# Kernel optimization log

Measured on AMD Instinct MI355X. Metric: run time of the kernel, lower is better.

The kernel has to match this reference:

```python
import jax, jax.numpy as jnp
import numpy as np

B, T, D, UNITS = 32, 2048, 1024, 1024


def setup_inputs() -> dict:
    key = jax.random.key(0)
    ks = jax.random.split(key, 9)
    values = jax.random.normal(ks[0], (B, T, D), dtype=jnp.float32)
    query = jax.random.normal(ks[1], (B, D), dtype=jnp.float32)
    # mask: 1.0 where position is masked out, 0.0 otherwise
    mask = jax.random.randint(ks[2], (B, T), 0, 2).astype(jnp.float32)
    # Dense params (keras Dense: y = x @ W + b)
    W1 = jax.random.normal(ks[3], (D, UNITS), dtype=jnp.float32) / np.sqrt(D)
    b1 = jnp.zeros((UNITS,), dtype=jnp.float32)
    W2 = jax.random.normal(ks[4], (D, UNITS), dtype=jnp.float32) / np.sqrt(D)
    b2 = jnp.zeros((UNITS,), dtype=jnp.float32)
    V = jax.random.normal(ks[5], (UNITS, 1), dtype=jnp.float32) / np.sqrt(UNITS)
    bV = jnp.zeros((1,), dtype=jnp.float32)
    return {"values": values, "query": query, "mask": mask,
            "W1": W1, "b1": b1, "W2": W2, "b2": b2, "V": V, "bV": bV}


def reference(values, query, mask, W1, b1, W2, b2, V, bV):
    # values: [B,T,D], query: [B,D], mask: [B,T] (1.0 = masked)
    proj_v = jnp.einsum('btd,du->btu', values, W1) + b1          # [B,T,U]
    proj_q = (query @ W2 + b2)[:, None, :]                        # [B,1,U]
    score = jnp.tanh(proj_v + proj_q) @ V + bV                    # [B,T,1]
    score = score + mask[:, :, None] * (-1e9)                     # mask out
    attention_weights = jax.nn.softmax(score, axis=1)             # [B,T,1]
    context_vector = jnp.sum(attention_weights * values, axis=1)  # [B,D]
    return (context_vector, attention_weights)
```

## Files before the change

### kernel.cpp

```cpp
#include <hip/hip_runtime.h>
#include <hip/hip_bf16.h>


typedef __bf16 bf16x8 __attribute__((ext_vector_type(8)));
typedef __bf16 bf16x4 __attribute__((ext_vector_type(4)));
typedef float  f32x4  __attribute__((ext_vector_type(4)));

#define B_  32
#define T_  2048
#define D_  1024
#define U_  1024
#define BT_ (B_*T_)

#define WS_W1T    ((size_t)0)
#define WS_PROJQ  ((size_t)(2u*1024*1024))
#define WS_SCORE  ((size_t)(2u*1024*1024 + 128u*1024))
#define WS_VALB   ((size_t)(4u*1024*1024))
#define WS_NEEDED (WS_VALB + (size_t)BT_ * D_ * 2)

__device__ __forceinline__ float tanh_fast(float x) {
    const float e = __expf(2.0f * x);
    return 1.0f - __fdividef(2.0f, e + 1.0f);
}

__device__ __forceinline__ void glls16(const void* g, void* l) {
    __builtin_amdgcn_global_load_lds(
        (const __attribute__((address_space(1))) void*)g,
        (__attribute__((address_space(3))) void*)l, 16, 0, 0);
}

__global__ void init_kernel(const float* __restrict__ b1, const float* __restrict__ b2,
                            float* __restrict__ projq, float* __restrict__ score) {
    int i = blockIdx.x * 256 + threadIdx.x;
    if (i < B_ * U_) {
        projq[i] = b1[i & (U_ - 1)] + b2[i & (U_ - 1)];
    } else {
        score[i - B_ * U_] = 0.0f;
    }
}

__global__ void convert_kernel(const float* __restrict__ v, __bf16* __restrict__ o) {
    const size_t i = ((size_t)blockIdx.x * 256 + threadIdx.x) * 8;
    const float4 a = *(const float4*)(v + i);
    const float4 b = *(const float4*)(v + i + 4);
    bf16x8 h;
    h[0] = (__bf16)a.x; h[1] = (__bf16)a.y; h[2] = (__bf16)a.z; h[3] = (__bf16)a.w;
    h[4] = (__bf16)b.x; h[5] = (__bf16)b.y; h[6] = (__bf16)b.z; h[7] = (__bf16)b.w;
    *(bf16x8*)(o + i) = h;
}

__global__ void w1_transpose_kernel(const float* __restrict__ W1, __bf16* __restrict__ W1T) {
    __shared__ float tile[64][65];
    const int bx = blockIdx.x & 15;
    const int by = blockIdx.x >> 4;
    const int tid = threadIdx.x;
    const int j  = tid & 63;
    const int i0 = tid >> 6;
#pragma unroll
    for (int p = 0; p < 16; ++p) {
        const int i = i0 + p * 4;
        tile[i][j] = W1[(size_t)(by * 64 + i) * U_ + bx * 64 + j];
    }
    __syncthreads();
#pragma unroll
    for (int p = 0; p < 16; ++p) {
        const int i = i0 + p * 4;
        W1T[(size_t)(bx * 64 + i) * D_ + by * 64 + j] = (__bf16)tile[j][i];
    }
}

__global__ void projq_kernel(const float* __restrict__ query, const float* __restrict__ W2,
                             float* __restrict__ projq) {
    __shared__ float q[128];
    const int b  = blockIdx.x >> 3;
    const int dc = blockIdx.x & 7;
    const int tid = threadIdx.x;
    if (tid < 128) q[tid] = query[(size_t)b * D_ + dc * 128 + tid];
    __syncthreads();
    const int u0 = tid * 4;
    float a0 = 0.f, a1 = 0.f, a2 = 0.f, a3 = 0.f;
    for (int d = 0; d < 128; ++d) {
        const float4 w = *(const float4*)(W2 + (size_t)(dc * 128 + d) * U_ + u0);
        const float qd = q[d];
        a0 = fmaf(qd, w.x, a0); a1 = fmaf(qd, w.y, a1);
        a2 = fmaf(qd, w.z, a2); a3 = fmaf(qd, w.w, a3);
    }
    float* p = projq + (size_t)b * U_ + u0;
    atomicAdd(p + 0, a0); atomicAdd(p + 1, a1);
    atomicAdd(p + 2, a2); atomicAdd(p + 3, a3);
}


#define SC_A_ELE 4096
#define SC_B_ELE 8192
#define SC_BUF   (SC_A_ELE + SC_B_ELE)

__global__ __launch_bounds__(512, 4)
void score_kernel_occ(const __bf16* __restrict__ valb, const __bf16* __restrict__ W1T,
                      const float* __restrict__ projq, const float* __restrict__ V,
                      float* __restrict__ score) {
    __shared__ __attribute__((aligned(16))) __bf16 lds[2 * SC_BUF];

    const int tid  = threadIdx.x;
    const int bid  = blockIdx.x;
    const int xcd  = bid & 7;
    const int sl   = bid >> 3;
    const int mblk = xcd * 64 + (sl >> 2);
    const int nblk = sl & 3;

    const int wv   = tid >> 6;
    const int lane = tid & 63;
    const int wm   = wv >> 2;
    const int wn   = wv & 3;
    const int l15  = lane & 15, quad = lane >> 4;

    const int rslot = (quad ^ ((l15 >> 1) & 3)) * 8;

    const int srow = lane >> 2;
    const int slog = ((lane & 3) ^ ((srow >> 1) & 3)) * 8;
    const __bf16* aS = valb + ((size_t)mblk * 128 + wv * 16 + srow) * D_ + slog;
    const __bf16* bS = W1T  + ((size_t)nblk * 256 + wv * 16 + srow) * D_ + slog;
    __bf16* aD = lds + wv * 512;
    __bf16* bD = lds + SC_A_ELE + wv * 512;

#define STAGE(CB, KT) do {                                                      \
    glls16(aS + (KT) * 32,                    aD + (CB));                       \
    glls16(bS + (KT) * 32,                    bD + (CB));                       \
    glls16(bS + (size_t)128 * D_ + (KT) * 32, bD + (CB) + 4096);                \
    } while (0)

#define BODY(KT, CB, DOS) do {                                                  \
    if (DOS) STAGE((CB) ^ SC_BUF, (KT) + 1);                                    \
    bf16x8 af[4], bf[4];                                                        \
    _Pragma("unroll")                                                           \
    for (int mt = 0; mt < 4; ++mt)                                              \
        af[mt] = *(const bf16x8*)(lds + (CB) +                                  \
                   (wm * 64 + mt * 16 + l15) * 32 + rslot);                     \
    _Pragma("unroll")                                                           \
    for (int nt = 0; nt < 4; ++nt)                                              \
        bf[nt] = *(const bf16x8*)(lds + (CB) + SC_A_ELE +                       \
                   (wn * 64 + nt * 16 + l15) * 32 + rslot);                     \
    _Pragma("unroll")                                                           \
    for (int nt = 0; nt < 4; ++nt)                                              \
    _Pragma("unroll")                                                           \
    for (int mt = 0; mt < 4; ++mt)                                              \
        acc[mt][nt] = __builtin_amdgcn_mfma_f32_16x16x32_bf16(                  \
            af[mt], bf[nt], acc[mt][nt], 0, 0, 0);                              \
    __syncthreads();                                                            \
    } while (0)

    f32x4 acc[4][4];
#pragma unroll
    for (int i = 0; i < 4; ++i)
#pragma unroll
        for (int j = 0; j < 4; ++j) { f32x4 z = {0.f, 0.f, 0.f, 0.f}; acc[i][j] = z; }

    STAGE(0, 0);
    __syncthreads();

#pragma unroll 1
    for (int kt = 0; kt < 32; kt += 2) {
        BODY(kt,     0,      1);
        BODY(kt + 1, SC_BUF, (kt + 1) < 31);
    }

    const int bq = mblk >> 4;
    const float* pq = projq + (size_t)bq * U_ + nblk * 256 + wn * 64;
    const float* Vp = V + nblk * 256 + wn * 64;
    float pqu[4], vu[4];
#pragma unroll
    for (int nt = 0; nt < 4; ++nt) { pqu[nt] = pq[nt * 16 + l15]; vu[nt] = Vp[nt * 16 + l15]; }
    const size_t rowbase = (size_t)mblk * 128 + (size_t)wm * 64;
#pragma unroll
    for (int mt = 0; mt < 4; ++mt) {
        float s0 = 0.f, s1 = 0.f, s2 = 0.f, s3 = 0.f;
#pragma unroll
        for (int nt = 0; nt < 4; ++nt) {
            s0 += tanh_fast(acc[mt][nt][0] + pqu[nt]) * vu[nt];
            s1 += tanh_fast(acc[mt][nt][1] + pqu[nt]) * vu[nt];
            s2 += tanh_fast(acc[mt][nt][2] + pqu[nt]) * vu[nt];
            s3 += tanh_fast(acc[mt][nt][3] + pqu[nt]) * vu[nt];
        }
        float s[4] = {s0, s1, s2, s3};
#pragma unroll
        for (int r = 0; r < 4; ++r) {
            float v = s[r];
            v += __shfl_xor(v, 1);
            v += __shfl_xor(v, 2);
            v += __shfl_xor(v, 4);
            v += __shfl_xor(v, 8);
            if (l15 == 0)
                atomicAdd(&score[rowbase + mt * 16 + quad * 4 + r], v);
        }
    }
#undef STAGE
#undef BODY
}

__global__ __launch_bounds__(512, 2)
void score_kernel_f32(const float* __restrict__ values, const __bf16* __restrict__ W1T,
                      const float* __restrict__ projq, const float* __restrict__ V,
                      float* __restrict__ score) {
    __shared__ __attribute__((aligned(16))) __bf16 Al[64][40];
    __shared__ __attribute__((aligned(16))) __bf16 Bl[512][40];
    const int tid    = threadIdx.x;
    const int rowblk = blockIdx.x >> 1;
    const int nhalf  = blockIdx.x & 1;
    const int wave = tid >> 6, lane = tid & 63;
    const int quad = lane >> 4, l15 = lane & 15;
    const float*  Abase = values + (size_t)rowblk * 64 * D_;
    const __bf16* Bbase = W1T + (size_t)nhalf * 512 * D_;
    const int ar = tid >> 3, ac = (tid & 7) * 4;
    const int br = tid >> 2, bc = (tid & 3) * 8;
    f32x4 acc[4][4];
#pragma unroll
    for (int i = 0; i < 4; ++i)
#pragma unroll
        for (int j = 0; j < 4; ++j) { f32x4 z = {0.f,0.f,0.f,0.f}; acc[i][j] = z; }
    for (int kk = 0; kk < D_; kk += 32) {
        {
            const float4 v = *(const float4*)(Abase + (size_t)ar * D_ + kk + ac);
            bf16x4 h;
            h[0] = (__bf16)v.x; h[1] = (__bf16)v.y; h[2] = (__bf16)v.z; h[3] = (__bf16)v.w;
            *(bf16x4*)(&Al[ar][ac]) = h;
        }
#pragma unroll
        for (int p = 0; p < 4; ++p) {
            const int rr = p * 128 + br;
            const bf16x8 w = *(const bf16x8*)(Bbase + (size_t)rr * D_ + kk + bc);
            *(bf16x8*)(&Bl[rr][bc]) = w;
        }
        __syncthreads();
        bf16x8 af[4];
#pragma unroll
        for (int mt = 0; mt < 4; ++mt)
            af[mt] = *(const bf16x8*)(&Al[mt * 16 + l15][quad * 8]);
#pragma unroll
        for (int nt = 0; nt < 4; ++nt) {
            const bf16x8 bfr = *(const bf16x8*)(&Bl[wave * 64 + nt * 16 + l15][quad * 8]);
#pragma unroll
            for (int mt = 0; mt < 4; ++mt)
                acc[mt][nt] = __builtin_amdgcn_mfma_f32_16x16x32_bf16(af[mt], bfr, acc[mt][nt], 0, 0, 0);
        }
        __syncthreads();
    }
    const int b = rowblk >> 5;
    const size_t rowbase = (size_t)rowblk * 64;
    const float* pq = projq + (size_t)b * U_;
    const int ub = nhalf * 512 + wave * 64;
#pragma unroll
    for (int mt = 0; mt < 4; ++mt) {
        float s0 = 0.f, s1 = 0.f, s2 = 0.f, s3 = 0.f;
#pragma unroll
        for (int nt = 0; nt < 4; ++nt) {
            const int u = ub + nt * 16 + l15;
            const float pqu = pq[u];
            const float vu  = V[u];
            s0 += tanh_fast(acc[mt][nt][0] + pqu) * vu;
            s1 += tanh_fast(acc[mt][nt][1] + pqu) * vu;
            s2 += tanh_fast(acc[mt][nt][2] + pqu) * vu;
            s3 += tanh_fast(acc[mt][nt][3] + pqu) * vu;
        }
        float s[4] = {s0, s1, s2, s3};
#pragma unroll
        for (int r = 0; r < 4; ++r) {
            float v = s[r];
            v += __shfl_xor(v, 1);
            v += __shfl_xor(v, 2);
            v += __shfl_xor(v, 4);
            v += __shfl_xor(v, 8);
            if (l15 == 0)
                atomicAdd(&score[rowbase + mt * 16 + quad * 4 + r], v);
        }
    }
}

__global__ void softmax_kernel(const float* __restrict__ score, const float* __restrict__ mask,
                               const float* __restrict__ bV, float* __restrict__ out) {
    const int b = blockIdx.x;
    const int tid = threadIdx.x;
    const float bv = bV[0];
    float s[8];
    float lmax = -3.0e38f;
#pragma unroll
    for (int i = 0; i < 8; ++i) {
        const int t = tid + i * 256;
        const float v = score[(size_t)b * T_ + t] + bv + mask[(size_t)b * T_ + t] * (-1.0e9f);
        s[i] = v;
        lmax = fmaxf(lmax, v);
    }
#pragma unroll
    for (int m = 1; m < 64; m <<= 1) lmax = fmaxf(lmax, __shfl_xor(lmax, m));
    __shared__ float redm[4], reds[4];
    if ((tid & 63) == 0) redm[tid >> 6] = lmax;
    __syncthreads();
    const float M = fmaxf(fmaxf(redm[0], redm[1]), fmaxf(redm[2], redm[3]));
    float lsum = 0.f;
#pragma unroll
    for (int i = 0; i < 8; ++i) { s[i] = __expf(s[i] - M); lsum += s[i]; }
#pragma unroll
    for (int m = 1; m < 64; m <<= 1) lsum += __shfl_xor(lsum, m);
    if ((tid & 63) == 0) reds[tid >> 6] = lsum;
    __syncthreads();
    const float inv = 1.0f / (reds[0] + reds[1] + reds[2] + reds[3]);
#pragma unroll
    for (int i = 0; i < 8; ++i)
        out[(size_t)B_ * D_ + (size_t)b * T_ + tid + i * 256] = s[i] * inv;
}

__global__ void context_kernel_bf16(const __bf16* __restrict__ valb, const float* __restrict__ attn,
                                    float* __restrict__ out) {
    const int b  = blockIdx.x >> 4;
    const int dc = blockIdx.x & 15;
    const int tid = threadIdx.x;
    __shared__ float a[T_];
#pragma unroll
    for (int i = 0; i < 8; ++i) a[tid + i * 256] = attn[(size_t)b * T_ + tid + i * 256];
    __syncthreads();
    const int dl = (tid & 7) * 8;
    const int tg = tid >> 3;
    const __bf16* vb = valb + (size_t)b * T_ * D_ + dc * 64 + dl;
    float acc[8];
#pragma unroll
    for (int j = 0; j < 8; ++j) acc[j] = 0.f;
#pragma unroll 4
    for (int t = tg; t < T_; t += 32) {
        const bf16x8 v = *(const bf16x8*)(vb + (size_t)t * D_);
        const float w = a[t];
#pragma unroll
        for (int j = 0; j < 8; ++j) acc[j] = fmaf(w, (float)v[j], acc[j]);
    }
    __shared__ __attribute__((aligned(16))) float red[32][65];
#pragma unroll
    for (int j = 0; j < 8; ++j) red[tg][dl + j] = acc[j];
    __syncthreads();
    if (tid < 64) {
        float s = 0.f;
#pragma unroll
        for (int g = 0; g < 32; ++g) s += red[g][tid];
        out[(size_t)b * D_ + dc * 64 + tid] = s;
    }
}

__global__ void context_kernel(const float* __restrict__ values, const float* __restrict__ attn,
                               float* __restrict__ out) {
    const int b  = blockIdx.x >> 4;
    const int dc = blockIdx.x & 15;
    const int tid = threadIdx.x;
    __shared__ float a[T_];
#pragma unroll
    for (int i = 0; i < 8; ++i) a[tid + i * 256] = attn[(size_t)b * T_ + tid + i * 256];
    __syncthreads();
    const int dl = (tid & 15) * 4;
    const int tg = tid >> 4;
    const float* vb = values + (size_t)b * T_ * D_ + dc * 64 + dl;
    f32x4 acc = {0.f, 0.f, 0.f, 0.f};
#pragma unroll 4
    for (int t = tg; t < T_; t += 16) {
        const float4 v = *(const float4*)(vb + (size_t)t * D_);
        const float w = a[t];
        acc[0] = fmaf(w, v.x, acc[0]);
        acc[1] = fmaf(w, v.y, acc[1]);
        acc[2] = fmaf(w, v.z, acc[2]);
        acc[3] = fmaf(w, v.w, acc[3]);
    }
    __shared__ __attribute__((aligned(16))) float red[16][64];
    *(f32x4*)(&red[tg][dl]) = acc;
    __syncthreads();
    if (tid < 64) {
        float s = 0.f;
#pragma unroll
        for (int g = 0; g < 16; ++g) s += red[g][tid];
        out[(size_t)b * D_ + dc * 64 + tid] = s;
    }
}

extern "C" void kernel_launch(void* const* d_in, const int* in_sizes, int n_in,
                              void* d_out, int out_size, void* d_ws, size_t ws_size,
                              hipStream_t stream) {
    const float* values = (const float*)d_in[0];
    const float* query  = (const float*)d_in[1];
    const float* mask   = (const float*)d_in[2];
    const float* W1     = (const float*)d_in[3];
    const float* b1     = (const float*)d_in[4];
    const float* W2     = (const float*)d_in[5];
    const float* b2     = (const float*)d_in[6];
    const float* V      = (const float*)d_in[7];
    const float* bV     = (const float*)d_in[8];
    float* out = (float*)d_out;

    char* ws = (char*)d_ws;
    __bf16* W1T   = (__bf16*)(ws + WS_W1T);
    float*  projq = (float*)(ws + WS_PROJQ);
    float*  score = (float*)(ws + WS_SCORE);
    __bf16* valb  = (__bf16*)(ws + WS_VALB);

    init_kernel<<<dim3(384), dim3(256), 0, stream>>>(b1, b2, projq, score);
    w1_transpose_kernel<<<dim3(256), dim3(256), 0, stream>>>(W1, W1T);
    projq_kernel<<<dim3(256), dim3(256), 0, stream>>>(query, W2, projq);
    if (ws_size >= WS_NEEDED) {
        convert_kernel<<<dim3(32768), dim3(256), 0, stream>>>(values, valb);
        score_kernel_occ<<<dim3(2048), dim3(512), 0, stream>>>(valb, W1T, projq, V, score);
        softmax_kernel<<<dim3(32), dim3(256), 0, stream>>>(score, mask, bV, out);
        context_kernel_bf16<<<dim3(512), dim3(256), 0, stream>>>(valb, out + B_ * D_, out);
    } else {
        score_kernel_f32<<<dim3(2048), dim3(512), 0, stream>>>(values, W1T, projq, V, score);
        softmax_kernel<<<dim3(32), dim3(256), 0, stream>>>(score, mask, bV, out);
        context_kernel<<<dim3(512), dim3(256), 0, stream>>>(values, out + B_ * D_, out);
    }
}
```

Before: 606.3 us.

## Triple-buffer score GEMM LDS staging with partial vmcnt waits

Moves the score GEMM from double to triple LDS buffering, prefetching two k-tiles ahead. The full __syncthreads is replaced by an explicit s_waitcnt vmcnt(3) and a raw s_barrier, so one tile's async loads can stay in flight across the barrier. This hides more global-load latency behind the MFMA work. The cost is 50% more LDS per block (72KB), which may cut the number of resident blocks below the launch bound of 4, and the hand-counted vmcnt depends on exactly three loads per stage.

```diff
diff --git a/kernel.cpp b/kernel.cpp
--- a/kernel.cpp
+++ b/kernel.cpp
@@ -93,13 +93,13 @@
 
 #define SC_A_ELE 4096
 #define SC_B_ELE 8192
-#define SC_BUF   (SC_A_ELE + SC_B_ELE)
+#define SC_BUFE  (SC_A_ELE + SC_B_ELE)
 
 __global__ __launch_bounds__(512, 4)
-void score_kernel_occ(const __bf16* __restrict__ valb, const __bf16* __restrict__ W1T,
-                      const float* __restrict__ projq, const float* __restrict__ V,
-                      float* __restrict__ score) {
-    __shared__ __attribute__((aligned(16))) __bf16 lds[2 * SC_BUF];
+void score_kernel_3buf(const __bf16* __restrict__ valb, const __bf16* __restrict__ W1T,
+                       const float* __restrict__ projq, const float* __restrict__ V,
+                       float* __restrict__ score) {
+    __shared__ __attribute__((aligned(16))) __bf16 lds[3 * SC_BUFE];
 
     const int tid  = threadIdx.x;
     const int bid  = blockIdx.x;
@@ -129,16 +129,16 @@
     glls16(bS + (size_t)128 * D_ + (KT) * 32, bD + (CB) + 4096);                \
     } while (0)
 
-#define BODY(KT, CB, DOS) do {                                                  \
-    if (DOS) STAGE((CB) ^ SC_BUF, (KT) + 1);                                    \
+#define STEP(KT, CBR, CBS, DOS, VM) do {                                        \
+    if (DOS) STAGE((CBS), (KT) + 2);                                            \
     bf16x8 af[4], bf[4];                                                        \
     _Pragma("unroll")                                                           \
     for (int mt = 0; mt < 4; ++mt)                                              \
-        af[mt] = *(const bf16x8*)(lds + (CB) +                                  \
+        af[mt] = *(const bf16x8*)(lds + (CBR) +                                 \
                    (wm * 64 + mt * 16 + l15) * 32 + rslot);                     \
     _Pragma("unroll")                                                           \
     for (int nt = 0; nt < 4; ++nt)                                              \
-        bf[nt] = *(const bf16x8*)(lds + (CB) + SC_A_ELE +                       \
+        bf[nt] = *(const bf16x8*)(lds + (CBR) + SC_A_ELE +                      \
                    (wn * 64 + nt * 16 + l15) * 32 + rslot);                     \
     _Pragma("unroll")                                                           \
     for (int nt = 0; nt < 4; ++nt)                                              \
@@ -146,7 +146,12 @@
     for (int mt = 0; mt < 4; ++mt)                                              \
         acc[mt][nt] = __builtin_amdgcn_mfma_f32_16x16x32_bf16(                  \
             af[mt], bf[nt], acc[mt][nt], 0, 0, 0);                              \
-    __syncthreads();                                                            \
+    if ((VM) >= 0) {                                                            \
+        if ((VM) == 3) asm volatile("s_waitcnt vmcnt(3)" ::: "memory");         \
+        else           asm volatile("s_waitcnt vmcnt(0)" ::: "memory");         \
+        __builtin_amdgcn_s_barrier();                                           \
+        asm volatile("" ::: "memory");                                          \
+    }                                                                           \
     } while (0)
 
     f32x4 acc[4][4];
@@ -156,13 +161,19 @@
         for (int j = 0; j < 4; ++j) { f32x4 z = {0.f, 0.f, 0.f, 0.f}; acc[i][j] = z; }
 
     STAGE(0, 0);
-    __syncthreads();
+    STAGE(SC_BUFE, 1);
+    asm volatile("s_waitcnt vmcnt(3)" ::: "memory");
+    __builtin_amdgcn_s_barrier();
+    asm volatile("" ::: "memory");
 
 #pragma unroll 1
-    for (int kt = 0; kt < 32; kt += 2) {
-        BODY(kt,     0,      1);
-        BODY(kt + 1, SC_BUF, (kt + 1) < 31);
-    }
+    for (int t = 0; t < 30; t += 3) {
+        STEP(t,     0,           2 * SC_BUFE, 1, 3);
+        STEP(t + 1, SC_BUFE,     0,           1, 3);
+        STEP(t + 2, 2 * SC_BUFE, SC_BUFE,     1, 3);
+    }
+    STEP(30, 0,       0, 0, 0);
+    STEP(31, SC_BUFE, 0, 0, -1);
 
     const int bq = mblk >> 4;
     const float* pq = projq + (size_t)bq * U_ + nblk * 256 + wn * 64;
@@ -194,7 +205,7 @@
         }
     }
 #undef STAGE
-#undef BODY
+#undef STEP
 }
 
 __global__ __launch_bounds__(512, 2)
@@ -400,7 +411,7 @@
     projq_kernel<<<dim3(256), dim3(256), 0, stream>>>(query, W2, projq);
     if (ws_size >= WS_NEEDED) {
         convert_kernel<<<dim3(32768), dim3(256), 0, stream>>>(values, valb);
-        score_kernel_occ<<<dim3(2048), dim3(512), 0, stream>>>(valb, W1T, projq, V, score);
+        score_kernel_3buf<<<dim3(2048), dim3(512), 0, stream>>>(valb, W1T, projq, V, score);
         softmax_kernel<<<dim3(32), dim3(256), 0, stream>>>(score, mask, bV, out);
         context_kernel_bf16<<<dim3(512), dim3(256), 0, stream>>>(valb, out + B_ * D_, out);
     } else {
```

Measured after the change: 593.3 us. 2.1% less time.

## Load W1 fragments directly from pre-tiled global layout, triple-buffer A in LDS

Applied to the files above, without the earlier changes.

Adds a transpose kernel that writes W1 in an MFMA-fragment-tiled bf16 layout, so the score GEMM loads B operands straight from global/L2 into registers instead of staging them through LDS. LDS now holds only the values tile, with a three-stage ring buffer and two tiles of prefetch. Explicit ds_read asm, waitcnt, sched barriers and setprio shape the schedule around the MFMAs. This cuts LDS traffic and footprint, at the cost of per-wave redundant global loads of W1 and raw-barrier synchronisation that relies on hand-placed waits.

```diff
diff --git a/kernel.cpp b/kernel.cpp
--- a/kernel.cpp
+++ b/kernel.cpp
@@ -4,6 +4,7 @@
 
 typedef __bf16 bf16x8 __attribute__((ext_vector_type(8)));
 typedef __bf16 bf16x4 __attribute__((ext_vector_type(4)));
+typedef short  s16x8  __attribute__((ext_vector_type(8)));
 typedef float  f32x4  __attribute__((ext_vector_type(4)));
 
 #define B_  32
@@ -49,6 +50,30 @@
     *(bf16x8*)(o + i) = h;
 }
 
+__global__ void w1_transpose_tiled_kernel(const float* __restrict__ W1, __bf16* __restrict__ W1TT) {
+    __shared__ float tile[64][65];
+    const int bx = blockIdx.x & 15;
+    const int by = blockIdx.x >> 4;
+    const int tid = threadIdx.x;
+    const int j  = tid & 63;
+    const int i0 = tid >> 6;
+#pragma unroll
+    for (int p = 0; p < 16; ++p) {
+        const int i = i0 + p * 4;
+        tile[i][j] = W1[(size_t)(by * 64 + i) * U_ + bx * 64 + j];
+    }
+    __syncthreads();
+#pragma unroll
+    for (int p = 0; p < 16; ++p) {
+        const int i = i0 + p * 4;
+        const int u = bx * 64 + i;
+        const int d = by * 64 + j;
+        const int idx = (((u >> 4) * 32 + (d >> 5)) * 512) +
+                        ((u & 15) * 4 + ((d >> 3) & 3)) * 8 + (d & 7);
+        W1TT[idx] = (__bf16)tile[j][i];
+    }
+}
+
 __global__ void w1_transpose_kernel(const float* __restrict__ W1, __bf16* __restrict__ W1T) {
     __shared__ float tile[64][65];
     const int bx = blockIdx.x & 15;
@@ -91,15 +116,13 @@
 }
 
 
-#define SC_A_ELE 4096
-#define SC_B_ELE 8192
-#define SC_BUF   (SC_A_ELE + SC_B_ELE)
+#define SC_ABUF 4096
 
 __global__ __launch_bounds__(512, 4)
-void score_kernel_occ(const __bf16* __restrict__ valb, const __bf16* __restrict__ W1T,
+void score_kernel_bl2(const __bf16* __restrict__ valb, const __bf16* __restrict__ W1TT,
                       const float* __restrict__ projq, const float* __restrict__ V,
                       float* __restrict__ score) {
-    __shared__ __attribute__((aligned(16))) __bf16 lds[2 * SC_BUF];
+    __shared__ __attribute__((aligned(16))) __bf16 lds[3 * SC_ABUF];
 
     const int tid  = threadIdx.x;
     const int bid  = blockIdx.x;
@@ -119,35 +142,39 @@
     const int srow = lane >> 2;
     const int slog = ((lane & 3) ^ ((srow >> 1) & 3)) * 8;
     const __bf16* aS = valb + ((size_t)mblk * 128 + wv * 16 + srow) * D_ + slog;
-    const __bf16* bS = W1T  + ((size_t)nblk * 256 + wv * 16 + srow) * D_ + slog;
     __bf16* aD = lds + wv * 512;
-    __bf16* bD = lds + SC_A_ELE + wv * 512;
-
-#define STAGE(CB, KT) do {                                                      \
-    glls16(aS + (KT) * 32,                    aD + (CB));                       \
-    glls16(bS + (KT) * 32,                    bD + (CB));                       \
-    glls16(bS + (size_t)128 * D_ + (KT) * 32, bD + (CB) + 4096);                \
-    } while (0)
-
-#define BODY(KT, CB, DOS) do {                                                  \
-    if (DOS) STAGE((CB) ^ SC_BUF, (KT) + 1);                                    \
-    bf16x8 af[4], bf[4];                                                        \
+
+    const __bf16* bB = W1TT + ((size_t)(nblk * 16 + wn * 4) * 32) * 512
+                            + (l15 * 4 + quad) * 8;
+
+#define DSR(dst, off) do { s16x8 _t;                                            \
+    asm volatile("ds_read_b128 %0, %1" : "=v"(_t)                              \
+        : "v"((const __attribute__((address_space(3))) __bf16*)(lds + (off)))); \
+    (dst) = __builtin_bit_cast(bf16x8, _t); } while (0)
+
+#define STEP(KT, CBR, CBS, DOS) do {                                            \
+    bf16x8 bf[4];                                                               \
+    _Pragma("unroll")                                                           \
+    for (int nt = 0; nt < 4; ++nt)                                              \
+        bf[nt] = *(const bf16x8*)(bB + ((size_t)(nt * 32 + (KT)) * 512));       \
+    __builtin_amdgcn_sched_barrier(0);                                          \
+    if (DOS) glls16(aS + ((KT) + 2) * 32, aD + (CBS));                          \
+    bf16x8 af[4];                                                               \
     _Pragma("unroll")                                                           \
     for (int mt = 0; mt < 4; ++mt)                                              \
-        af[mt] = *(const bf16x8*)(lds + (CB) +                                  \
-                   (wm * 64 + mt * 16 + l15) * 32 + rslot);                     \
-    _Pragma("unroll")                                                           \
-    for (int nt = 0; nt < 4; ++nt)                                              \
-        bf[nt] = *(const bf16x8*)(lds + (CB) + SC_A_ELE +                       \
-                   (wn * 64 + nt * 16 + l15) * 32 + rslot);                     \
+        DSR(af[mt], (CBR) + (wm * 64 + mt * 16 + l15) * 32 + rslot);            \
+    asm volatile("s_waitcnt lgkmcnt(0)" ::: "memory");                          \
+    __builtin_amdgcn_sched_barrier(0);                                          \
+    __builtin_amdgcn_s_setprio(1);                                              \
     _Pragma("unroll")                                                           \
     for (int nt = 0; nt < 4; ++nt)                                              \
     _Pragma("unroll")                                                           \
     for (int mt = 0; mt < 4; ++mt)                                              \
         acc[mt][nt] = __builtin_amdgcn_mfma_f32_16x16x32_bf16(                  \
             af[mt], bf[nt], acc[mt][nt], 0, 0, 0);                              \
-    __syncthreads();                                                            \
-    } while (0)
+    __builtin_amdgcn_s_setprio(0);                                              \
+    __builtin_amdgcn_s_barrier();                                               \
+} while (0)
 
     f32x4 acc[4][4];
 #pragma unroll
@@ -155,14 +182,19 @@
 #pragma unroll
         for (int j = 0; j < 4; ++j) { f32x4 z = {0.f, 0.f, 0.f, 0.f}; acc[i][j] = z; }
 
-    STAGE(0, 0);
-    __syncthreads();
+    glls16(aS + 0,  aD + 0);
+    glls16(aS + 32, aD + SC_ABUF);
+    asm volatile("s_waitcnt vmcnt(1)" ::: "memory");
+    __builtin_amdgcn_s_barrier();
 
 #pragma unroll 1
-    for (int kt = 0; kt < 32; kt += 2) {
-        BODY(kt,     0,      1);
-        BODY(kt + 1, SC_BUF, (kt + 1) < 31);
-    }
+    for (int t = 0; t < 30; t += 3) {
+        STEP(t,     0,           2 * SC_ABUF, 1);
+        STEP(t + 1, SC_ABUF,     0,           1);
+        STEP(t + 2, 2 * SC_ABUF, SC_ABUF,     1);
+    }
+    STEP(30, 0,       0, 0);
+    STEP(31, SC_ABUF, 0, 0);
 
     const int bq = mblk >> 4;
     const float* pq = projq + (size_t)bq * U_ + nblk * 256 + wn * 64;
@@ -193,8 +225,8 @@
                 atomicAdd(&score[rowbase + mt * 16 + quad * 4 + r], v);
         }
     }
-#undef STAGE
-#undef BODY
+#undef DSR
+#undef STEP
 }
 
 __global__ __launch_bounds__(512, 2)
@@ -396,14 +428,15 @@
     __bf16* valb  = (__bf16*)(ws + WS_VALB);
 
     init_kernel<<<dim3(384), dim3(256), 0, stream>>>(b1, b2, projq, score);
-    w1_transpose_kernel<<<dim3(256), dim3(256), 0, stream>>>(W1, W1T);
     projq_kernel<<<dim3(256), dim3(256), 0, stream>>>(query, W2, projq);
     if (ws_size >= WS_NEEDED) {
+        w1_transpose_tiled_kernel<<<dim3(256), dim3(256), 0, stream>>>(W1, W1T);
         convert_kernel<<<dim3(32768), dim3(256), 0, stream>>>(values, valb);
-        score_kernel_occ<<<dim3(2048), dim3(512), 0, stream>>>(valb, W1T, projq, V, score);
+        score_kernel_bl2<<<dim3(2048), dim3(512), 0, stream>>>(valb, W1T, projq, V, score);
         softmax_kernel<<<dim3(32), dim3(256), 0, stream>>>(score, mask, bV, out);
         context_kernel_bf16<<<dim3(512), dim3(256), 0, stream>>>(valb, out + B_ * D_, out);
     } else {
+        w1_transpose_kernel<<<dim3(256), dim3(256), 0, stream>>>(W1, W1T);
         score_kernel_f32<<<dim3(2048), dim3(512), 0, stream>>>(values, W1T, projq, V, score);
         softmax_kernel<<<dim3(32), dim3(256), 0, stream>>>(score, mask, bV, out);
         context_kernel<<<dim3(512), dim3(256), 0, stream>>>(values, out + B_ * D_, out);
```

Measured after the change: 625.8 us. 3.2% more time.
